# Kernel tuning notes

Hardware: AMD Instinct MI355X
Metric: run time of the kernel (lower is better)

The kernel has to match this reference:

```python
import jax, jax.numpy as jnp
import numpy as np

B, N, H, C = 64, 307, 64, 12   # batch, nodes, hidden_channels, input_channels
D = H * C                       # GATv2 out_channels = hidden*input
E = 2456                        # number of (random) graph edges
NEG_SLOPE = 0.2


def setup_inputs() -> dict:
    key = jax.random.key(0)
    ks = jax.random.split(key, 8)
    sW = 1.0 / np.sqrt(H)
    sA = 1.0 / np.sqrt(D)
    return {
        "t": 0,
        "z": jax.random.normal(ks[0], (B * N, H), jnp.float32),
        "r1": jax.random.randint(ks[1], (E,), 0, N),
        "r2": jax.random.randint(ks[2], (E,), 0, N),
        "Wl": (jax.random.normal(ks[3], (H, D), jnp.float32) * sW),
        "bl": jnp.zeros((D,), jnp.float32),
        "Wr": (jax.random.normal(ks[4], (H, D), jnp.float32) * sW),
        "br": jnp.zeros((D,), jnp.float32),
        "att": (jax.random.normal(ks[5], (D,), jnp.float32) * sA),
        "bias": jnp.zeros((D,), jnp.float32),
    }


def _gatv2_batched(x, src, dst, Wl, bl, Wr, br, att, bias):
    # x: [B, N, H]; identical topology for all batch samples, so the
    # per-sample Python loop in the original collapses to one batched pass.
    xl = jnp.einsum("bnh,hd->nbd", x, Wl) + bl  # [N, B, D]  (lin_l, messages)
    xr = jnp.einsum("bnh,hd->nbd", x, Wr) + br  # [N, B, D]  (lin_r, targets)
    h = xl[src] + xr[dst]                        # [E+N, B, D]
    e = jnp.einsum("ebd,d->eb", jax.nn.leaky_relu(h, NEG_SLOPE), att)  # [E+N, B]
    # edge softmax over incoming edges of each target node (dst)
    emax = jax.ops.segment_max(e, dst, num_segments=N)   # [N, B]
    ee = jnp.exp(e - emax[dst])
    denom = jax.ops.segment_sum(ee, dst, num_segments=N)  # [N, B]
    alpha = ee / denom[dst]                                # [E+N, B]
    out = jax.ops.segment_sum(alpha[:, :, None] * xl[src], dst, num_segments=N)
    return out + bias                                      # [N, B, D]


def reference(t, z, r1, r2, Wl, bl, Wr, br, att, bias):
    x = z.reshape(B, N, H)
    # PyG GATv2Conv with add_self_loops=True: append one self loop per node.
    loops = jnp.arange(N)
    src = jnp.concatenate([r1, loops])
    dst = jnp.concatenate([r2, loops])
    out = _gatv2_batched(x, src, dst, Wl, bl, Wr, br, att, bias)  # [N, B, D]
    out = out.transpose(1, 0, 2)          # [B, N, D]
    return out.reshape(B * N, H, C)
```

## Files before the change

### kernel.cpp

```cpp
#include <hip/hip_runtime.h>

#define BB 64
#define NN 307
#define HH 64
#define DD 768
#define EE 2456
#define ET 2763
#define MM (BB*NN)
#define DEGMAX 128
#define SEGCAP 48
#define NG 77

#define XL_OFF   0u
#define XL_SZ    (MM*DD*2u)
#define XR_OFF   (XL_OFF + XL_SZ)
#define GSRC_OFF (XR_OFF + XL_SZ)
#define GDEG_OFF (GSRC_OFF + NN*DEGMAX*4u)

typedef __attribute__((ext_vector_type(8))) _Float16 half8;
typedef __attribute__((ext_vector_type(2))) _Float16 h2;
typedef __attribute__((ext_vector_type(4))) float f32x4;
typedef __attribute__((ext_vector_type(2))) float f32x2;
typedef __attribute__((ext_vector_type(4))) unsigned u32x4;
typedef __attribute__((ext_vector_type(2))) unsigned u32x2;

#if defined(__has_builtin)
#if __has_builtin(__builtin_amdgcn_fdot2)
#define HAS_FDOT2 1
#endif
#endif

__device__ __forceinline__ unsigned short f2h(float f){
  union{_Float16 h; unsigned short u;} c; c.h = (_Float16)f; return c.u;
}
__device__ __forceinline__ h2 u2h(unsigned u){
  union{unsigned u; h2 h;} c; c.u = u; return c.h;
}

__global__ __launch_bounds__(256) void k_gemm(
    const float* __restrict__ z,
    const float* __restrict__ Wl, const float* __restrict__ bl,
    const float* __restrict__ Wr, const float* __restrict__ br,
    const int* __restrict__ r1, const int* __restrict__ r2,
    int* __restrict__ gdeg, int* __restrict__ gsrc,
    unsigned short* __restrict__ xl, unsigned short* __restrict__ xr)
{
  __shared__ unsigned short sBTl[128][72];
  __shared__ unsigned short sBTr[128][72];
  __shared__ unsigned short sC[64][136];
  __shared__ int sseg[4][SEGCAP];
  __shared__ int scnt[4];

  const int tid = threadIdx.x;
  const int lane = tid & 63, wv = tid >> 6;

  if (blockIdx.z == 1){
    if (blockIdx.y >= 2) return;
    const int n = (int)blockIdx.y * 154 + (int)blockIdx.x;
    if (n >= NN) return;
    const int W = (ET + 3) / 4;
    const int e0 = wv * W;
    const int e1 = (e0 + W < ET) ? e0 + W : ET;
    int cnt = 0;
    for (int base = e0; base < e1; base += 64){
      int e = base + lane;
      int d = -1, s = 0;
      if (e < e1){
        if (e < EE){ d = r2[e]; s = r1[e]; }
        else       { d = e - EE; s = d; }
      }
      bool hit = (d == n);
      unsigned long long mb = __ballot(hit);
      if (hit){
        int pos = cnt + (int)__popcll(mb & ((1ull << lane) - 1ull));
        if (pos < SEGCAP) sseg[wv][pos] = s;
      }
      cnt += (int)__popcll(mb);
    }
    if (lane == 0) scnt[wv] = (cnt < SEGCAP) ? cnt : SEGCAP;
    __syncthreads();
    int c0 = scnt[0], c1 = scnt[1], c2 = scnt[2], c3 = scnt[3];
    int off = (wv > 0 ? c0 : 0) + (wv > 1 ? c1 : 0) + (wv > 2 ? c2 : 0);
    int cw = scnt[wv];
    int deg = c0 + c1 + c2 + c3;
    if (lane < cw && off + lane < DEGMAX) gsrc[n*DEGMAX + off + lane] = sseg[wv][lane];
    if (tid == 0) gdeg[n] = (deg < DEGMAX) ? deg : DEGMAX;
    return;
  }

  const int n0 = blockIdx.y*128;

  #pragma unroll
  for (int it=0; it<32; it++){
    int idx = it*256 + tid;
    int k = idx >> 7, c = idx & 127;
    sBTl[c][k] = f2h(Wl[(size_t)k*DD + n0 + c]);
    sBTr[c][k] = f2h(Wr[(size_t)k*DD + n0 + c]);
  }

  const int bcol = lane & 15;
  const int kp   = (lane >> 4) * 8;

  #pragma unroll 1
  for (int t=0; t<2; t++){
    const int tm = (int)blockIdx.x*2 + t;
    if (tm >= MM/64) break;
    const int m0 = tm*64;

    const int arow = m0 + wv*16 + (lane & 15);
    const float* pz = z + (size_t)arow*HH + kp;
    float4 za0 = *(const float4*)(pz);
    float4 za1 = *(const float4*)(pz + 4);
    float4 zb0 = *(const float4*)(pz + 32);
    float4 zb1 = *(const float4*)(pz + 36);
    half8 a0, a1;
    a0[0]=(_Float16)za0.x; a0[1]=(_Float16)za0.y; a0[2]=(_Float16)za0.z; a0[3]=(_Float16)za0.w;
    a0[4]=(_Float16)za1.x; a0[5]=(_Float16)za1.y; a0[6]=(_Float16)za1.z; a0[7]=(_Float16)za1.w;
    a1[0]=(_Float16)zb0.x; a1[1]=(_Float16)zb0.y; a1[2]=(_Float16)zb0.z; a1[3]=(_Float16)zb0.w;
    a1[4]=(_Float16)zb1.x; a1[5]=(_Float16)zb1.y; a1[6]=(_Float16)zb1.z; a1[7]=(_Float16)zb1.w;
    __syncthreads();

    f32x4 accl[8], accr[8];
    #pragma unroll
    for (int cb=0; cb<8; cb++){
      accl[cb][0]=0.f; accl[cb][1]=0.f; accl[cb][2]=0.f; accl[cb][3]=0.f;
      accr[cb][0]=0.f; accr[cb][1]=0.f; accr[cb][2]=0.f; accr[cb][3]=0.f;
    }

    #pragma unroll
    for (int cb=0; cb<8; cb++){
      half8 b0l = *(const half8*)&sBTl[cb*16 + bcol][kp];
      half8 b1l = *(const half8*)&sBTl[cb*16 + bcol][32 + kp];
      accl[cb] = __builtin_amdgcn_mfma_f32_16x16x32_f16(a0, b0l, accl[cb], 0, 0, 0);
      accl[cb] = __builtin_amdgcn_mfma_f32_16x16x32_f16(a1, b1l, accl[cb], 0, 0, 0);
      half8 b0r = *(const half8*)&sBTr[cb*16 + bcol][kp];
      half8 b1r = *(const half8*)&sBTr[cb*16 + bcol][32 + kp];
      accr[cb] = __builtin_amdgcn_mfma_f32_16x16x32_f16(a0, b0r, accr[cb], 0, 0, 0);
      accr[cb] = __builtin_amdgcn_mfma_f32_16x16x32_f16(a1, b1r, accr[cb], 0, 0, 0);
    }

    #pragma unroll
    for (int cb=0; cb<8; cb++){
      int cc = cb*16 + bcol;
      float bb = bl[n0 + cc];
      #pragma unroll
      for (int r=0; r<4; r++){
        int rr = wv*16 + (lane>>4)*4 + r;
        sC[rr][cc] = f2h(accl[cb][r] + bb);
      }
    }
    __syncthreads();
    #pragma unroll
    for (int it=0; it<4; it++){
      int idx = it*256 + tid;
      int rr = idx >> 4;
      int c8 = (idx & 15) * 8;
      uint4 v = *(const uint4*)&sC[rr][c8];
      *(uint4*)&xl[(size_t)(m0+rr)*DD + n0 + c8] = v;
    }
    __syncthreads();
    #pragma unroll
    for (int cb=0; cb<8; cb++){
      int cc = cb*16 + bcol;
      float bb = br[n0 + cc];
      #pragma unroll
      for (int r=0; r<4; r++){
        int rr = wv*16 + (lane>>4)*4 + r;
        sC[rr][cc] = f2h(accr[cb][r] + bb);
      }
    }
    __syncthreads();
    #pragma unroll
    for (int it=0; it<4; it++){
      int idx = it*256 + tid;
      int rr = idx >> 4;
      int c8 = (idx & 15) * 8;
      uint4 v = *(const uint4*)&sC[rr][c8];
      *(uint4*)&xr[(size_t)(m0+rr)*DD + n0 + c8] = v;
    }
  }
}


template<int CTRL, int RM>
__device__ __forceinline__ float dpp_add(float v){
  int x = __builtin_amdgcn_update_dpp(0, __float_as_int(v), CTRL, RM, 0xf, true);
  return v + __int_as_float(x);
}
__device__ __forceinline__ float redux64s(float v){
  v = dpp_add<0x121,0xf>(v);
  v = dpp_add<0x122,0xf>(v);
  v = dpp_add<0x124,0xf>(v);
  v = dpp_add<0x128,0xf>(v);
  v = dpp_add<0x142,0xa>(v);
  v = dpp_add<0x143,0x8>(v);
  return __uint_as_float((unsigned)__builtin_amdgcn_readlane(__float_as_int(v), 63));
}

#define LOAD6(DST, P) {                                           \
  u32x4 _u0 = *(const u32x4*)((P) + duA);                         \
  u32x2 _u1 = *(const u32x2*)((P) + duB);                         \
  DST[0]=_u0.x; DST[1]=_u0.y; DST[2]=_u0.z; DST[3]=_u0.w;         \
  DST[4]=_u1.x; DST[5]=_u1.y; }

#define READS(J) __builtin_amdgcn_readlane((((J) & 64) ? sv1 : sv0), (J) & 63)
#define EADDR(J)  ((const unsigned*)(xlb + (size_t)READS(J)*DD))
#define EADDRC(J) ({ int _q = (J); int _qc = _q < degm1 ? _q : degm1;  \
                     (const unsigned*)(xlb + (size_t)READS(_qc)*DD); })

#define MKH(H, U) {                                               \
  _Pragma("unroll")                                               \
  for (int _t=0;_t<6;_t++) H[_t] = u2h(U[_t]) + xrh[_t]; }

#ifdef HAS_FDOT2
#define SCORE(S, H) {                                             \
  _Pragma("unroll")                                               \
  for (int _t=0;_t<6;_t++){                                       \
    h2 _l = __builtin_elementwise_max(H[_t], H[_t]*c02h);         \
    S = __builtin_amdgcn_fdot2(_l, atth[_t], S, false); } }
#else
#define SCORE(S, H) {                                             \
  _Pragma("unroll")                                               \
  for (int _t=0;_t<6;_t++){                                       \
    h2 _l = __builtin_elementwise_max(H[_t], H[_t]*c02h);         \
    S += (float)_l[0]*(float)atth[_t][0] + (float)_l[1]*(float)atth[_t][1]; } }
#endif

#define ACCH(P, H) {                                              \
  _Pragma("unroll")                                               \
  for (int _t=0;_t<6;_t++){                                       \
    acc2[_t].x += (P) * (float)H[_t][0];                          \
    acc2[_t].y += (P) * (float)H[_t][1]; } }

#define STEP1R(U, C, JN) {                                        \
  h2 hU[6];                                                       \
  MKH(hU, U);                                                     \
  if (C) LOAD6(U, EADDRC(JN));                                    \
  float sU = 0.f;                                                 \
  SCORE(sU, hU);                                                  \
  float scU = redux64s(sU);                                       \
  float pU = __builtin_amdgcn_exp2f(scU - C2);                    \
  ssum += pU;                                                     \
  ACCH(pU, hU); }

__global__ __launch_bounds__(256) void k_fusedf(
    const unsigned short* __restrict__ xl, const unsigned short* __restrict__ xr,
    const int* __restrict__ gdeg, const int* __restrict__ gsrc,
    const float* __restrict__ att, const float* __restrict__ bias,
    float* __restrict__ out)
{
  const unsigned id = blockIdx.x;
  const int xcd = (int)(id & 7u);
  const unsigned k = id >> 3;
  const int b = xcd + 8 * (int)(k / NG);
  const int g = (int)(k % NG);
  const int wv = threadIdx.x >> 6;
  const int nv = g*4 + wv;
  if (nv >= NN) return;
  const int n = __builtin_amdgcn_readfirstlane(nv);
  const int lane = threadIdx.x & 63;
  const int duA = lane * 4;
  const int duB = 256 + lane * 2;

  int sv0 = gsrc[n*DEGMAX + lane];
  int sv1 = gsrc[n*DEGMAX + 64 + lane];
  const int deg = __builtin_amdgcn_readfirstlane(gdeg[n]);
  const int degm1 = deg - 1;

  const unsigned short* xlb = xl + (size_t)b*NN*DD;

  unsigned uA[6], uB[6], uC[6], uD[6];
  LOAD6(uA, EADDR(0));
  LOAD6(uB, EADDRC(1));
  LOAD6(uC, EADDRC(2));
  LOAD6(uD, EADDRC(3));

  h2 atth[6], xrh[6];
  const h2 c02h = {(_Float16)0.2f, (_Float16)0.2f};
  {
    const f32x2* paA = (const f32x2*)(att) + lane*4;
    const f32x2* paB = (const f32x2*)(att + 512) + lane*2;
    #pragma unroll
    for (int t=0;t<4;t++){
      f32x2 a = paA[t];
      atth[t][0] = (_Float16)(a.x * 1.4426950408889634f);
      atth[t][1] = (_Float16)(a.y * 1.4426950408889634f);
    }
    #pragma unroll
    for (int t=0;t<2;t++){
      f32x2 a = paB[t];
      atth[4+t][0] = (_Float16)(a.x * 1.4426950408889634f);
      atth[4+t][1] = (_Float16)(a.y * 1.4426950408889634f);
    }
    const unsigned* px = (const unsigned*)(xr + ((size_t)b*NN + n)*DD);
    u32x4 x0 = __builtin_nontemporal_load((const u32x4*)(px + duA));
    u32x2 x1 = __builtin_nontemporal_load((const u32x2*)(px + duB));
    xrh[0] = u2h(x0.x); xrh[1] = u2h(x0.y); xrh[2] = u2h(x0.z);
    xrh[3] = u2h(x0.w); xrh[4] = u2h(x1.x); xrh[5] = u2h(x1.y);
  }
  f32x2 acc2[6];
  #pragma unroll
  for (int t=0;t<6;t++){ acc2[t].x = 0.f; acc2[t].y = 0.f; }

  float ssum = 0.f;
  const float C2 = 11.5415603f;

  int i = 0;
  for (; i + 4 <= deg; i += 4){
    const bool more = (i + 4 < deg);
    STEP1R(uA, more, i+4);
    STEP1R(uB, more, i+5);
    STEP1R(uC, more, i+6);
    STEP1R(uD, more, i+7);
  }
  {
    const int rem = deg - i;
    if (rem >= 1) STEP1R(uA, false, 0);
    if (rem >= 2) STEP1R(uB, false, 0);
    if (rem == 3) STEP1R(uC, false, 0);
  }

  const float inv = 1.f / ssum;
  float* po = out + ((size_t)b*NN + n)*DD;
  const f32x2* pbA = (const f32x2*)(bias) + lane*4;
  const f32x2* pbB = (const f32x2*)(bias + 512) + lane*2;
  f32x2 pb[6];
  #pragma unroll
  for (int t=0;t<4;t++) pb[t] = pbA[t];
  #pragma unroll
  for (int t=0;t<2;t++) pb[4+t] = pbB[t];

  f32x2 o2[6];
  #pragma unroll
  for (int t=0;t<6;t++){
    o2[t].x = acc2[t].x * inv + (pb[t].x - (float)xrh[t][0]);
    o2[t].y = acc2[t].y * inv + (pb[t].y - (float)xrh[t][1]);
  }
  {
    f32x4 oa; oa[0]=o2[0].x; oa[1]=o2[0].y; oa[2]=o2[1].x; oa[3]=o2[1].y;
    f32x4 ob; ob[0]=o2[2].x; ob[1]=o2[2].y; ob[2]=o2[3].x; ob[3]=o2[3].y;
    f32x4 oc; oc[0]=o2[4].x; oc[1]=o2[4].y; oc[2]=o2[5].x; oc[3]=o2[5].y;
    __builtin_nontemporal_store(oa, (f32x4*)(po + lane*8));
    __builtin_nontemporal_store(ob, (f32x4*)(po + lane*8 + 4));
    __builtin_nontemporal_store(oc, (f32x4*)(po + 512 + lane*4));
  }
}

extern "C" void kernel_launch(void* const* d_in, const int* in_sizes, int n_in,
                              void* d_out, int out_size, void* d_ws, size_t ws_size,
                              hipStream_t stream)
{
  const float* z   = (const float*)d_in[1];
  const int*   r1  = (const int*)  d_in[2];
  const int*   r2  = (const int*)  d_in[3];
  const float* Wl  = (const float*)d_in[4];
  const float* bl  = (const float*)d_in[5];
  const float* Wr  = (const float*)d_in[6];
  const float* br  = (const float*)d_in[7];
  const float* att = (const float*)d_in[8];
  const float* bias= (const float*)d_in[9];
  float* out = (float*)d_out;

  char* ws = (char*)d_ws;
  unsigned short* xl = (unsigned short*)(ws + XL_OFF);
  unsigned short* xr = (unsigned short*)(ws + XR_OFF);
  int* gsrc = (int*)(ws + GSRC_OFF);
  int* gdeg = (int*)(ws + GDEG_OFF);

  k_gemm<<<dim3((MM/64 + 1)/2, DD/128, 2), 256, 0, stream>>>(z, Wl, bl, Wr, br,
                                                     r1, r2, gdeg, gsrc, xl, xr);
  k_fusedf<<<dim3(8*8*NG, 1, 1), 256, 0, stream>>>(xl, xr, gdeg, gsrc, att, bias, out);
}
```

Before: 59.23 us.

## Precast inputs to fp16 in a prep kernel and shrink gather prefetch depth

```diff
diff --git a/kernel.cpp b/kernel.cpp
--- a/kernel.cpp
+++ b/kernel.cpp
@@ -16,6 +16,9 @@
 #define XR_OFF   (XL_OFF + XL_SZ)
 #define GSRC_OFF (XR_OFF + XL_SZ)
 #define GDEG_OFF (GSRC_OFF + NN*DEGMAX*4u)
+#define ZH_OFF   ((GDEG_OFF + NN*4u + 63u) & ~63u)
+#define WLH_OFF  (ZH_OFF + MM*HH*2u)
+#define WRH_OFF  (WLH_OFF + HH*DD*2u)
 
 typedef __attribute__((ext_vector_type(8))) _Float16 half8;
 typedef __attribute__((ext_vector_type(2))) _Float16 h2;
@@ -23,6 +26,7 @@
 typedef __attribute__((ext_vector_type(2))) float f32x2;
 typedef __attribute__((ext_vector_type(4))) unsigned u32x4;
 typedef __attribute__((ext_vector_type(2))) unsigned u32x2;
+typedef __attribute__((ext_vector_type(4))) unsigned short us4;
 
 #if defined(__has_builtin)
 #if __has_builtin(__builtin_amdgcn_fdot2)
@@ -37,10 +41,33 @@
   union{unsigned u; h2 h;} c; c.u = u; return c.h;
 }
 
+#define NZ8 ((MM*HH)/8)
+#define NW8 ((HH*DD)/8)
+
+__global__ __launch_bounds__(256) void k_prep(
+    const float* __restrict__ z, const float* __restrict__ Wl,
+    const float* __restrict__ Wr,
+    unsigned short* __restrict__ zh, unsigned short* __restrict__ wlh,
+    unsigned short* __restrict__ wrh)
+{
+  const int tid = (int)blockIdx.x*256 + (int)threadIdx.x;
+  const float* src; unsigned short* dst; int t;
+  if (tid < NZ8){ src = z;  dst = zh;  t = tid; }
+  else if (tid < NZ8 + NW8){ src = Wl; dst = wlh; t = tid - NZ8; }
+  else if (tid < NZ8 + 2*NW8){ src = Wr; dst = wrh; t = tid - NZ8 - NW8; }
+  else return;
+  const float4* p = (const float4*)(src + (size_t)t*8);
+  float4 a = p[0], b = p[1];
+  us4 o0 = { f2h(a.x), f2h(a.y), f2h(a.z), f2h(a.w) };
+  us4 o1 = { f2h(b.x), f2h(b.y), f2h(b.z), f2h(b.w) };
+  *(us4*)(dst + (size_t)t*8)     = o0;
+  *(us4*)(dst + (size_t)t*8 + 4) = o1;
+}
+
 __global__ __launch_bounds__(256) void k_gemm(
-    const float* __restrict__ z,
-    const float* __restrict__ Wl, const float* __restrict__ bl,
-    const float* __restrict__ Wr, const float* __restrict__ br,
+    const unsigned short* __restrict__ zh,
+    const unsigned short* __restrict__ wlh, const float* __restrict__ bl,
+    const unsigned short* __restrict__ wrh, const float* __restrict__ br,
     const int* __restrict__ r1, const int* __restrict__ r2,
     int* __restrict__ gdeg, int* __restrict__ gsrc,
     unsigned short* __restrict__ xl, unsigned short* __restrict__ xr)
@@ -91,11 +118,16 @@
   const int n0 = blockIdx.y*128;
 
   #pragma unroll
-  for (int it=0; it<32; it++){
+  for (int it=0; it<16; it++){
     int idx = it*256 + tid;
-    int k = idx >> 7, c = idx & 127;
-    sBTl[c][k] = f2h(Wl[(size_t)k*DD + n0 + c]);
-    sBTr[c][k] = f2h(Wr[(size_t)k*DD + n0 + c]);
+    int k  = idx >> 6;
+    int c2 = idx & 63;
+    unsigned ul = *(const unsigned*)(wlh + (size_t)k*DD + n0 + c2*2);
+    unsigned ur = *(const unsigned*)(wrh + (size_t)k*DD + n0 + c2*2);
+    sBTl[c2*2  ][k] = (unsigned short)(ul & 0xffffu);
+    sBTl[c2*2+1][k] = (unsigned short)(ul >> 16);
+    sBTr[c2*2  ][k] = (unsigned short)(ur & 0xffffu);
+    sBTr[c2*2+1][k] = (unsigned short)(ur >> 16);
   }
 
   const int bcol = lane & 15;
@@ -108,16 +140,9 @@
     const int m0 = tm*64;
 
     const int arow = m0 + wv*16 + (lane & 15);
-    const float* pz = z + (size_t)arow*HH + kp;
-    float4 za0 = *(const float4*)(pz);
-    float4 za1 = *(const float4*)(pz + 4);
-    float4 zb0 = *(const float4*)(pz + 32);
-    float4 zb1 = *(const float4*)(pz + 36);
-    half8 a0, a1;
-    a0[0]=(_Float16)za0.x; a0[1]=(_Float16)za0.y; a0[2]=(_Float16)za0.z; a0[3]=(_Float16)za0.w;
-    a0[4]=(_Float16)za1.x; a0[5]=(_Float16)za1.y; a0[6]=(_Float16)za1.z; a0[7]=(_Float16)za1.w;
-    a1[0]=(_Float16)zb0.x; a1[1]=(_Float16)zb0.y; a1[2]=(_Float16)zb0.z; a1[3]=(_Float16)zb0.w;
-    a1[4]=(_Float16)zb1.x; a1[5]=(_Float16)zb1.y; a1[6]=(_Float16)zb1.z; a1[7]=(_Float16)zb1.w;
+    const unsigned short* pz = zh + (size_t)arow*HH + kp;
+    half8 a0 = *(const half8*)(pz);
+    half8 a1 = *(const half8*)(pz + 32);
     __syncthreads();
 
     f32x4 accl[8], accr[8];
@@ -269,11 +294,10 @@
 
   const unsigned short* xlb = xl + (size_t)b*NN*DD;
 
-  unsigned uA[6], uB[6], uC[6], uD[6];
+  unsigned uA[6], uB[6], uC[6];
   LOAD6(uA, EADDR(0));
   LOAD6(uB, EADDRC(1));
   LOAD6(uC, EADDRC(2));
-  LOAD6(uD, EADDRC(3));
 
   h2 atth[6], xrh[6];
   const h2 c02h = {(_Float16)0.2f, (_Float16)0.2f};
@@ -306,18 +330,16 @@
   const float C2 = 11.5415603f;
 
   int i = 0;
-  for (; i + 4 <= deg; i += 4){
-    const bool more = (i + 4 < deg);
-    STEP1R(uA, more, i+4);
-    STEP1R(uB, more, i+5);
-    STEP1R(uC, more, i+6);
-    STEP1R(uD, more, i+7);
+  for (; i + 3 <= deg; i += 3){
+    const bool more = (i + 3 < deg);
+    STEP1R(uA, more, i+3);
+    STEP1R(uB, more, i+4);
+    STEP1R(uC, more, i+5);
   }
   {
     const int rem = deg - i;
     if (rem >= 1) STEP1R(uA, false, 0);
-    if (rem >= 2) STEP1R(uB, false, 0);
-    if (rem == 3) STEP1R(uC, false, 0);
+    if (rem == 2) STEP1R(uB, false, 0);
   }
 
   const float inv = 1.f / ssum;
@@ -362,12 +384,17 @@
   float* out = (float*)d_out;
 
   char* ws = (char*)d_ws;
-  unsigned short* xl = (unsigned short*)(ws + XL_OFF);
-  unsigned short* xr = (unsigned short*)(ws + XR_OFF);
+  unsigned short* xl  = (unsigned short*)(ws + XL_OFF);
+  unsigned short* xr  = (unsigned short*)(ws + XR_OFF);
   int* gsrc = (int*)(ws + GSRC_OFF);
   int* gdeg = (int*)(ws + GDEG_OFF);
-
-  k_gemm<<<dim3((MM/64 + 1)/2, DD/128, 2), 256, 0, stream>>>(z, Wl, bl, Wr, br,
+  unsigned short* zh  = (unsigned short*)(ws + ZH_OFF);
+  unsigned short* wlh = (unsigned short*)(ws + WLH_OFF);
+  unsigned short* wrh = (unsigned short*)(ws + WRH_OFF);
+
+  k_prep<<<dim3((NZ8 + 2*NW8 + 255)/256, 1, 1), 256, 0, stream>>>(
+      z, Wl, Wr, zh, wlh, wrh);
+  k_gemm<<<dim3((MM/64 + 1)/2, DD/128, 2), 256, 0, stream>>>(zh, wlh, bl, wrh, br,
                                                      r1, r2, gdeg, gsrc, xl, xr);
   k_fusedf<<<dim3(8*8*NG, 1, 1), 256, 0, stream>>>(xl, xr, gdeg, gsrc, att, bias, out);
 }
```

After: 64.47 us. 8.8% more time.

## Process two target nodes per wavefront with interleaved edge gathers

Applied to the files above, without the earlier changes.

```diff
diff --git a/kernel.cpp b/kernel.cpp
--- a/kernel.cpp
+++ b/kernel.cpp
@@ -9,7 +9,7 @@
 #define MM (BB*NN)
 #define DEGMAX 128
 #define SEGCAP 48
-#define NG 77
+#define NGP 39
 
 #define XL_OFF   0u
 #define XL_SZ    (MM*DD*2u)
@@ -99,7 +99,7 @@
   }
 
   const int bcol = lane & 15;
-  const int kp   = (lane >> 4) * 8;
+  const int kp   = (lane >> 6 ? 0 : (lane >> 4) * 8);
 
   #pragma unroll 1
   for (int t=0; t<2; t++){
@@ -203,14 +203,13 @@
   DST[0]=_u0.x; DST[1]=_u0.y; DST[2]=_u0.z; DST[3]=_u0.w;         \
   DST[4]=_u1.x; DST[5]=_u1.y; }
 
-#define READS(J) __builtin_amdgcn_readlane((((J) & 64) ? sv1 : sv0), (J) & 63)
-#define EADDR(J)  ((const unsigned*)(xlb + (size_t)READS(J)*DD))
-#define EADDRC(J) ({ int _q = (J); int _qc = _q < degm1 ? _q : degm1;  \
-                     (const unsigned*)(xlb + (size_t)READS(_qc)*DD); })
-
-#define MKH(H, U) {                                               \
+#define READS2(S0, S1, J) __builtin_amdgcn_readlane((((J) & 64) ? (S1) : (S0)), (J) & 63)
+#define EADDR2(S0, S1, J, DM) ({ int _q = (J); int _qc = _q < (DM) ? _q : (DM); \
+    (const unsigned*)(xlb + (size_t)READS2(S0, S1, _qc)*DD); })
+
+#define MKH2(H, U, XR) {                                          \
   _Pragma("unroll")                                               \
-  for (int _t=0;_t<6;_t++) H[_t] = u2h(U[_t]) + xrh[_t]; }
+  for (int _t=0;_t<6;_t++) H[_t] = u2h(U[_t]) + XR[_t]; }
 
 #ifdef HAS_FDOT2
 #define SCORE(S, H) {                                             \
@@ -226,22 +225,25 @@
     S += (float)_l[0]*(float)atth[_t][0] + (float)_l[1]*(float)atth[_t][1]; } }
 #endif
 
-#define ACCH(P, H) {                                              \
+#define ACCH2(A, P, H) {                                          \
   _Pragma("unroll")                                               \
   for (int _t=0;_t<6;_t++){                                       \
-    acc2[_t].x += (P) * (float)H[_t][0];                          \
-    acc2[_t].y += (P) * (float)H[_t][1]; } }
-
-#define STEP1R(U, C, JN) {                                        \
-  h2 hU[6];                                                       \
-  MKH(hU, U);                                                     \
-  if (C) LOAD6(U, EADDRC(JN));                                    \
-  float sU = 0.f;                                                 \
-  SCORE(sU, hU);                                                  \
-  float scU = redux64s(sU);                                       \
-  float pU = __builtin_amdgcn_exp2f(scU - C2);                    \
-  ssum += pU;                                                     \
-  ACCH(pU, hU); }
+    A[_t].x += (P) * (float)H[_t][0];                             \
+    A[_t].y += (P) * (float)H[_t][1]; } }
+
+#define STEPP(U0, U1, JC, C, JN) {                                \
+  h2 h0_[6], h1_[6];                                              \
+  MKH2(h0_, U0, xrh0); MKH2(h1_, U1, xrh1);                       \
+  if (C){ LOAD6(U0, EADDR2(sa0, sa1, (JN), dA));                  \
+          LOAD6(U1, EADDR2(sb0, sb1, (JN), dB)); }                \
+  float s0_ = 0.f, s1_ = 0.f;                                     \
+  SCORE(s0_, h0_); SCORE(s1_, h1_);                               \
+  float sc0_ = redux64s(s0_);                                     \
+  float sc1_ = redux64s(s1_);                                     \
+  float p0_ = ((JC) < deg0) ? __builtin_amdgcn_exp2f(sc0_ - C2) : 0.f; \
+  float p1_ = ((JC) < deg1) ? __builtin_amdgcn_exp2f(sc1_ - C2) : 0.f; \
+  ssum0 += p0_; ssum1 += p1_;                                     \
+  ACCH2(acc0, p0_, h0_); ACCH2(acc1, p1_, h1_); }
 
 __global__ __launch_bounds__(256) void k_fusedf(
     const unsigned short* __restrict__ xl, const unsigned short* __restrict__ xr,
@@ -252,30 +254,38 @@
   const unsigned id = blockIdx.x;
   const int xcd = (int)(id & 7u);
   const unsigned k = id >> 3;
-  const int b = xcd + 8 * (int)(k / NG);
-  const int g = (int)(k % NG);
+  const int b = xcd + 8 * (int)(k / NGP);
+  const int g = (int)(k % NGP);
   const int wv = threadIdx.x >> 6;
-  const int nv = g*4 + wv;
-  if (nv >= NN) return;
-  const int n = __builtin_amdgcn_readfirstlane(nv);
+  const int n0v = g*8 + wv*2;
+  if (n0v >= NN) return;
+  const int n0 = __builtin_amdgcn_readfirstlane(n0v);
+  const int has1 = (n0 + 1 < NN);
+  const int n1 = has1 ? n0 + 1 : n0;
   const int lane = threadIdx.x & 63;
   const int duA = lane * 4;
   const int duB = 256 + lane * 2;
 
-  int sv0 = gsrc[n*DEGMAX + lane];
-  int sv1 = gsrc[n*DEGMAX + 64 + lane];
-  const int deg = __builtin_amdgcn_readfirstlane(gdeg[n]);
-  const int degm1 = deg - 1;
+  int sa0 = gsrc[n0*DEGMAX + lane];
+  int sa1 = gsrc[n0*DEGMAX + 64 + lane];
+  int sb0 = gsrc[n1*DEGMAX + lane];
+  int sb1 = gsrc[n1*DEGMAX + 64 + lane];
+  const int deg0 = __builtin_amdgcn_readfirstlane(gdeg[n0]);
+  int d1t = __builtin_amdgcn_readfirstlane(gdeg[n1]);
+  const int deg1 = has1 ? d1t : 0;
+  const int dm = deg0 > deg1 ? deg0 : deg1;
+  const int dA = deg0 - 1;
+  const int dB = (deg1 > 0) ? deg1 - 1 : 0;
 
   const unsigned short* xlb = xl + (size_t)b*NN*DD;
 
-  unsigned uA[6], uB[6], uC[6], uD[6];
-  LOAD6(uA, EADDR(0));
-  LOAD6(uB, EADDRC(1));
-  LOAD6(uC, EADDRC(2));
-  LOAD6(uD, EADDRC(3));
-
-  h2 atth[6], xrh[6];
+  unsigned uA0[6], uA1[6], uB0[6], uB1[6];
+  LOAD6(uA0, EADDR2(sa0, sa1, 0, dA));
+  LOAD6(uA1, EADDR2(sb0, sb1, 0, dB));
+  LOAD6(uB0, EADDR2(sa0, sa1, 1, dA));
+  LOAD6(uB1, EADDR2(sb0, sb1, 1, dB));
+
+  h2 atth[6], xrh0[6], xrh1[6];
   const h2 c02h = {(_Float16)0.2f, (_Float16)0.2f};
   {
     const f32x2* paA = (const f32x2*)(att) + lane*4;
@@ -292,36 +302,35 @@
       atth[4+t][0] = (_Float16)(a.x * 1.4426950408889634f);
       atth[4+t][1] = (_Float16)(a.y * 1.4426950408889634f);
     }
-    const unsigned* px = (const unsigned*)(xr + ((size_t)b*NN + n)*DD);
-    u32x4 x0 = __builtin_nontemporal_load((const u32x4*)(px + duA));
-    u32x2 x1 = __builtin_nontemporal_load((const u32x2*)(px + duB));
-    xrh[0] = u2h(x0.x); xrh[1] = u2h(x0.y); xrh[2] = u2h(x0.z);
-    xrh[3] = u2h(x0.w); xrh[4] = u2h(x1.x); xrh[5] = u2h(x1.y);
-  }
-  f32x2 acc2[6];
+    const unsigned* px0 = (const unsigned*)(xr + ((size_t)b*NN + n0)*DD);
+    u32x4 x0 = __builtin_nontemporal_load((const u32x4*)(px0 + duA));
+    u32x2 x1 = __builtin_nontemporal_load((const u32x2*)(px0 + duB));
+    xrh0[0] = u2h(x0.x); xrh0[1] = u2h(x0.y); xrh0[2] = u2h(x0.z);
+    xrh0[3] = u2h(x0.w); xrh0[4] = u2h(x1.x); xrh0[5] = u2h(x1.y);
+    const unsigned* px1 = (const unsigned*)(xr + ((size_t)b*NN + n1)*DD);
+    u32x4 y0 = __builtin_nontemporal_load((const u32x4*)(px1 + duA));
+    u32x2 y1 = __builtin_nontemporal_load((const u32x2*)(px1 + duB));
+    xrh1[0] = u2h(y0.x); xrh1[1] = u2h(y0.y); xrh1[2] = u2h(y0.z);
+    xrh1[3] = u2h(y0.w); xrh1[4] = u2h(y1.x); xrh1[5] = u2h(y1.y);
+  }
+  f32x2 acc0[6], acc1[6];
   #pragma unroll
-  for (int t=0;t<6;t++){ acc2[t].x = 0.f; acc2[t].y = 0.f; }
-
-  float ssum = 0.f;
+  for (int t=0;t<6;t++){
+    acc0[t].x = 0.f; acc0[t].y = 0.f;
+    acc1[t].x = 0.f; acc1[t].y = 0.f;
+  }
+
+  float ssum0 = 0.f, ssum1 = 0.f;
   const float C2 = 11.5415603f;
 
-  int i = 0;
-  for (; i + 4 <= deg; i += 4){
-    const bool more = (i + 4 < deg);
-    STEP1R(uA, more, i+4);
-    STEP1R(uB, more, i+5);
-    STEP1R(uC, more, i+6);
-    STEP1R(uD, more, i+7);
-  }
-  {
-    const int rem = deg - i;
-    if (rem >= 1) STEP1R(uA, false, 0);
-    if (rem >= 2) STEP1R(uB, false, 0);
-    if (rem == 3) STEP1R(uC, false, 0);
-  }
-
-  const float inv = 1.f / ssum;
-  float* po = out + ((size_t)b*NN + n)*DD;
+  int j = 0;
+  for (; j + 2 <= dm; j += 2){
+    const bool more = (j + 2 < dm);
+    STEPP(uA0, uA1, j,   more, j+2);
+    STEPP(uB0, uB1, j+1, more, j+3);
+  }
+  if (j < dm) STEPP(uA0, uA1, j, false, 0);
+
   const f32x2* pbA = (const f32x2*)(bias) + lane*4;
   const f32x2* pbB = (const f32x2*)(bias + 512) + lane*2;
   f32x2 pb[6];
@@ -330,13 +339,31 @@
   #pragma unroll
   for (int t=0;t<2;t++) pb[4+t] = pbB[t];
 
-  f32x2 o2[6];
-  #pragma unroll
-  for (int t=0;t<6;t++){
-    o2[t].x = acc2[t].x * inv + (pb[t].x - (float)xrh[t][0]);
-    o2[t].y = acc2[t].y * inv + (pb[t].y - (float)xrh[t][1]);
-  }
   {
+    const float inv = 1.f / ssum0;
+    float* po = out + ((size_t)b*NN + n0)*DD;
+    f32x2 o2[6];
+    #pragma unroll
+    for (int t=0;t<6;t++){
+      o2[t].x = acc0[t].x * inv + (pb[t].x - (float)xrh0[t][0]);
+      o2[t].y = acc0[t].y * inv + (pb[t].y - (float)xrh0[t][1]);
+    }
+    f32x4 oa; oa[0]=o2[0].x; oa[1]=o2[0].y; oa[2]=o2[1].x; oa[3]=o2[1].y;
+    f32x4 ob; ob[0]=o2[2].x; ob[1]=o2[2].y; ob[2]=o2[3].x; ob[3]=o2[3].y;
+    f32x4 oc; oc[0]=o2[4].x; oc[1]=o2[4].y; oc[2]=o2[5].x; oc[3]=o2[5].y;
+    __builtin_nontemporal_store(oa, (f32x4*)(po + lane*8));
+    __builtin_nontemporal_store(ob, (f32x4*)(po + lane*8 + 4));
+    __builtin_nontemporal_store(oc, (f32x4*)(po + 512 + lane*4));
+  }
+  if (has1){
+    const float inv = 1.f / ssum1;
+    float* po = out + ((size_t)b*NN + n1)*DD;
+    f32x2 o2[6];
+    #pragma unroll
+    for (int t=0;t<6;t++){
+      o2[t].x = acc1[t].x * inv + (pb[t].x - (float)xrh1[t][0]);
+      o2[t].y = acc1[t].y * inv + (pb[t].y - (float)xrh1[t][1]);
+    }
     f32x4 oa; oa[0]=o2[0].x; oa[1]=o2[0].y; oa[2]=o2[1].x; oa[3]=o2[1].y;
     f32x4 ob; ob[0]=o2[2].x; ob[1]=o2[2].y; ob[2]=o2[3].x; ob[3]=o2[3].y;
     f32x4 oc; oc[0]=o2[4].x; oc[1]=o2[4].y; oc[2]=o2[5].x; oc[3]=o2[5].y;
@@ -369,5 +396,5 @@
 
   k_gemm<<<dim3((MM/64 + 1)/2, DD/128, 2), 256, 0, stream>>>(z, Wl, bl, Wr, br,
                                                      r1, r2, gdeg, gsrc, xl, xr);
-  k_fusedf<<<dim3(8*8*NG, 1, 1), 256, 0, stream>>>(xl, xr, gdeg, gsrc, att, bias, out);
-}
+  k_fusedf<<<dim3(8*8*NGP, 1, 1), 256, 0, stream>>>(xl, xr, gdeg, gsrc, att, bias, out);
+}
```

Measured after the change: 66.08 us. 1.12x slower.
